# Kernel tuning notes

Measured on AMD Instinct MI355X. Metric: run time of the kernel, lower is better.

The kernel has to match this reference:

```python
import jax, jax.numpy as jnp
import numpy as np

SAMPLE_POINTS = 1000
THRESH = 0.1
MAX_RATIO = 0.1
BIG = 1e9


def _sobel_boundary(mask):
    # mask: [B, H, W] -> boundary magnitude [B, H, W]
    kx = jnp.array([[-1, 0, 1], [-2, 0, 2], [-1, 0, 1]], jnp.float32).reshape(1, 1, 3, 3)
    ky = jnp.array([[-1, -2, -1], [0, 0, 0], [1, 2, 1]], jnp.float32).reshape(1, 1, 3, 3)
    x = mask[:, None, :, :]
    dn = ('NCHW', 'OIHW', 'NCHW')
    gx = jax.lax.conv_general_dilated(x, kx, (1, 1), [(1, 1), (1, 1)], dimension_numbers=dn)
    gy = jax.lax.conv_general_dilated(x, ky, (1, 1), [(1, 1), (1, 1)], dimension_numbers=dn)
    return jnp.sqrt(gx * gx + gy * gy + 1e-8)[:, 0]


def _extract_points(bmap, keys, H, W):
    # bmap: [B, H, W]. Returns points [B, P, 2] float and validity mask [B, P].
    # Torch version uses torch.where + randperm subsampling; here we pick a
    # uniformly-random subset of valid boundary pixels via noisy top_k
    # (fixed-shape, jit-compatible stream compaction).
    def one(bm, key):
        flat = bm.reshape(-1)
        valid = flat > THRESH
        noise = jax.random.uniform(key, flat.shape)
        score = valid.astype(jnp.float32) * 2.0 + noise  # valid in (2,3), invalid in (0,1)
        _, idx = jax.lax.top_k(score, SAMPLE_POINTS)
        pts = jnp.stack([(idx // W).astype(jnp.float32), (idx % W).astype(jnp.float32)], axis=-1)
        pvalid = valid[idx]
        has_any = valid.any()
        # empty-boundary fallback: single center point (like torch version)
        center = jnp.array([H // 2, W // 2], jnp.float32)
        pts = jnp.where(has_any, pts, jnp.broadcast_to(center, pts.shape))
        pvalid = jnp.where(has_any, pvalid, jnp.arange(SAMPLE_POINTS) == 0)
        return pts, pvalid

    return jax.vmap(one)(bmap, keys)


def _hausdorff(pp, pv, tp, tv, diag):
    # pp: [B,P,2], tp: [B,T,2]; masked symmetric Hausdorff per batch element.
    pp2 = jnp.sum(pp * pp, -1)  # [B,P]
    tp2 = jnp.sum(tp * tp, -1)  # [B,T]
    d2 = pp2[:, :, None] + tp2[:, None, :] - 2.0 * jnp.einsum('bpc,btc->bpt', pp, tp)
    D = jnp.sqrt(jnp.maximum(d2, 0.0))  # [B,P,T]
    min_p2t = jnp.min(jnp.where(tv[:, None, :], D, BIG), axis=2)  # [B,P]
    a = jnp.max(jnp.where(pv, min_p2t, -BIG), axis=1)  # [B]
    min_t2p = jnp.min(jnp.where(pv[:, :, None], D, BIG), axis=1)  # [B,T]
    b = jnp.max(jnp.where(tv, min_t2p, -BIG), axis=1)  # [B]
    hd = jnp.maximum(a, b) / diag
    return jnp.clip(hd, 0.0, MAX_RATIO)


def setup_inputs() -> dict:
    key = jax.random.key(0)
    k1, k2 = jax.random.split(key)
    B, H, W = 64, 512, 512
    pred_logits = jax.random.normal(k1, (B, H, W), dtype=jnp.float32)
    target = (jax.random.uniform(k2, (B, H, W)) > 0.5).astype(jnp.float32)
    return {"pred_logits": pred_logits, "target": target}


def reference(pred_logits, target):
    B, H, W = pred_logits.shape
    pred_probs = jax.nn.sigmoid(pred_logits)
    bmap_pred = _sobel_boundary(pred_probs)
    bmap_tgt = _sobel_boundary(target)
    keys = jax.random.split(jax.random.key(1), 2 * B)
    pp, pv = _extract_points(bmap_pred, keys[:B], H, W)
    tp, tv = _extract_points(bmap_tgt, keys[B:], H, W)
    diag = jnp.sqrt(jnp.float32(H * H + W * W))
    hd = _hausdorff(pp, pv, tp, tv, diag)  # [B]
    return jnp.mean(hd)
```

## Files before the change

kernel.cpp:

```cpp
#include <hip/hip_runtime.h>
#include <stdint.h>


#define HH 512
#define WW 512
#define NPIX (HH * WW)
#define NSEL 1000
#define SLICE_CAP 320
#define CUTM (253u << 14)
#define BITCUT ((((253u << 15) - 1u)) << 9)
#define ROWS_PER 32

#if __has_builtin(__builtin_amdgcn_alignbit)
__device__ __forceinline__ uint32_t rotl32(uint32_t x, int r) {
  return __builtin_amdgcn_alignbit(x, x, (32 - r) & 31);
}
#else
__device__ __forceinline__ uint32_t rotl32(uint32_t x, int r) {
  return (x << r) | (x >> (32 - r));
}
#endif

template <int R>
__device__ __forceinline__ uint32_t rotlT(uint32_t x) {
  uint32_t d;
  asm("v_alignbit_b32 %0, %1, %1, %2" : "=v"(d) : "v"(x), "n"(32 - R));
  return d;
}

__device__ __forceinline__ void tf2x32(uint32_t k0, uint32_t k1,
                                       uint32_t c0, uint32_t c1,
                                       uint32_t& o0, uint32_t& o1) {
  uint32_t ks2 = k0 ^ k1 ^ 0x1BD11BDAu;
  uint32_t x0 = c0 + k0, x1 = c1 + k1;
#define TF_R(r) { x0 += x1; x1 = rotl32(x1, (r)); x1 ^= x0; }
  TF_R(13) TF_R(15) TF_R(26) TF_R(6)
  x0 += k1;  x1 += ks2 + 1u;
  TF_R(17) TF_R(29) TF_R(16) TF_R(24)
  x0 += ks2; x1 += k0 + 2u;
  TF_R(13) TF_R(15) TF_R(26) TF_R(6)
  x0 += k0;  x1 += k1 + 3u;
  TF_R(17) TF_R(29) TF_R(16) TF_R(24)
  x0 += k1;  x1 += ks2 + 4u;
  TF_R(13) TF_R(15) TF_R(26) TF_R(6)
  x0 += ks2; x1 += k0 + 5u;
#undef TF_R
  o0 = x0; o1 = x1;
}

__device__ __forceinline__ uint32_t m_from_bits(uint32_t bits) {
  float noise = __uint_as_float((bits >> 9) | 0x3F800000u) - 1.0f;
  float score = 2.0f + noise;
  return __float_as_uint(score) - 0x40000000u;
}

__device__ __forceinline__ uint32_t pixel_m(uint32_t k0, uint32_t k1, int p) {
  uint32_t b1, b2;
  tf2x32(k0, k1, 0u, (uint32_t)p, b1, b2);
  return m_from_bits(b1 ^ b2);
}

__device__ __forceinline__ float sigf(float x) { return 1.0f / (1.0f + __expf(-x)); }

__device__ __forceinline__ float ldval(const float* __restrict__ img, int r, int c, bool isPred) {
  if (r < 0 || r > HH - 1 || c < 0 || c > WW - 1) return 0.0f;
  float v = img[(size_t)r * WW + c];
  return isPred ? sigf(v) : v;
}

__device__ __forceinline__ uint32_t pack_pt(uint32_t p) {
  return ((p >> 9) << 16) | (p & 511u);
}

template <bool PRED>
__device__ __forceinline__ void sobel_body(const float* __restrict__ img, int b,
                                           int slice, int t,
                                           unsigned long long* stage, int* s_cn,
                                           int* s_cv) {
  const int lane = t & 63, w = t >> 6;
  const int rbase = slice * ROWS_PER + 8 * w;
  uint32_t k0, k1;
  tf2x32(0u, 1u, 0u, (uint32_t)b, k0, k1);
  k0 = __builtin_amdgcn_readfirstlane(k0);
  k1 = __builtin_amdgcn_readfirstlane(k1);
  const uint32_t ks2 = k0 ^ k1 ^ 0x1BD11BDAu;

  float P[10], Q[10], R[10];
  float4 na, nb;
  int cnt = 0;
  const uint32_t pbase = (uint32_t)((rbase << 9) + (lane << 3));

  auto issue = [&](int rn) {
    if ((unsigned)rn < (unsigned)HH) {
      const float* rp = img + ((size_t)rn << 9) + (lane << 3);
      na = *(const float4*)rp;
      nb = *(const float4*)(rp + 4);
    }
  };
  auto promote = [&](float (&vv)[10], int rn) {
    if ((unsigned)rn < (unsigned)HH) {
      float4 x = na, y = nb;
      if (PRED) {
        x.x = sigf(x.x); x.y = sigf(x.y); x.z = sigf(x.z); x.w = sigf(x.w);
        y.x = sigf(y.x); y.y = sigf(y.y); y.z = sigf(y.z); y.w = sigf(y.w);
      }
      vv[1] = x.x; vv[2] = x.y; vv[3] = x.z; vv[4] = x.w;
      vv[5] = y.x; vv[6] = y.y; vv[7] = y.z; vv[8] = y.w;
      float l = __shfl_up(y.w, 1);
      float r = __shfl_down(x.x, 1);
      vv[0] = (lane == 0) ? 0.0f : l;
      vv[9] = (lane == 63) ? 0.0f : r;
    } else {
#pragma unroll
      for (int i = 0; i < 10; ++i) vv[i] = 0.0f;
    }
  };

  issue(rbase - 1); promote(P, rbase - 1);
  issue(rbase);     promote(Q, rbase);
  issue(rbase + 1);

#pragma unroll 1
  for (int r = 0; r < 8; ++r) {
    promote(R, rbase + r + 1);
    if (r < 7) issue(rbase + r + 2);
    __builtin_amdgcn_sched_barrier(0);

    const uint32_t prow = pbase + ((uint32_t)r << 9);
    uint32_t X0[8], X1[8];
    const uint32_t pk = prow + k1;
    const uint32_t s0 = pk + k0;
#pragma unroll
    for (int j = 0; j < 8; ++j) {
      uint32_t x1i = pk + (uint32_t)j;
      X0[j] = s0 + (uint32_t)j;
      X1[j] = rotlT<13>(x1i) ^ X0[j];
    }
#define RND(rr)                                                         \
  _Pragma("unroll") for (int j = 0; j < 8; ++j) {                       \
    X0[j] += X1[j];                                                     \
    X1[j] = rotlT<(rr)>(X1[j]) ^ X0[j];                                 \
  }
#define INJ(ka, kb, i)                                                  \
  _Pragma("unroll") for (int j = 0; j < 8; ++j) {                       \
    X0[j] += (ka);                                                      \
    X1[j] += (kb) + (uint32_t)(i);                                      \
  }
    RND(15) RND(26) RND(6)  INJ(k1, ks2, 1)
    RND(17) RND(29) RND(16) RND(24) INJ(ks2, k0, 2)
    RND(13) RND(15) RND(26) RND(6)  INJ(k0, k1, 3)
    RND(17) RND(29) RND(16) RND(24) INJ(k1, ks2, 4)
    RND(13) RND(15) RND(26) RND(6)  INJ(ks2, k0, 5)
#undef RND
#undef INJ
    uint32_t bits[8];
#pragma unroll
    for (int j = 0; j < 8; ++j) bits[j] = X0[j] ^ X1[j];

    float da[10], e[10];
#pragma unroll
    for (int k = 0; k < 10; ++k) {
      da[k] = R[k] - P[k];
      e[k] = P[k] + 2.0f * Q[k] + R[k];
    }
    uint32_t candmask = 0;
#pragma unroll
    for (int j = 0; j < 8; ++j) {
      float gx = e[j + 2] - e[j];
      float gy = da[j] + 2.0f * da[j + 1] + da[j + 2];
      bool vld = (gx * gx + gy * gy + 1e-8f) > 0.01f;
      cnt += vld ? 1 : 0;
      candmask |= ((vld && bits[j] >= BITCUT) ? 1u : 0u) << j;
    }
    if (candmask) {
      int base = atomicAdd(s_cn, __popc(candmask));
      do {
        int j = __ffs(candmask) - 1;
        candmask &= candmask - 1;
        if (base < SLICE_CAP) {
          uint32_t m = m_from_bits(bits[j]);
          stage[base] = ((unsigned long long)m << 32) | (prow + (uint32_t)j);
        }
        ++base;
      } while (candmask);
    }
#pragma unroll
    for (int k = 0; k < 10; ++k) { P[k] = Q[k]; Q[k] = R[k]; }
  }
#pragma unroll
  for (int o = 32; o > 0; o >>= 1) cnt += __shfl_down(cnt, o);
  if (lane == 0) atomicAdd(s_cv, cnt);
}

__global__ __launch_bounds__(256, 8) void sobel_cand(
    const float* __restrict__ pred, const float* __restrict__ tgt,
    int2* __restrict__ g_scnt, unsigned long long* __restrict__ g_cand,
    uint32_t* __restrict__ g_hmax, int* __restrict__ g_done) {
  const int bid = blockIdx.x;
  const int b = bid >> 4, s = bid & 15;
  const int t = threadIdx.x;
  __shared__ unsigned long long stage[SLICE_CAP];
  __shared__ int s_cn, s_cv;
  if (t == 0) { s_cn = 0; s_cv = 0; }
  if (bid == 0) {
    if (t < 64) g_hmax[t] = 0u;
    if (t == 64) *g_done = 0;
  }
  __syncthreads();
  if (b < 64) sobel_body<true>(pred + (size_t)b * NPIX, b, s, t, stage, &s_cn, &s_cv);
  else        sobel_body<false>(tgt + (size_t)(b - 64) * NPIX, b, s, t, stage, &s_cn, &s_cv);
  __syncthreads();
  const int raw = s_cn;
  const int n = raw < SLICE_CAP ? raw : SLICE_CAP;
  for (int i = t; i < n; i += 256) g_cand[(size_t)bid * SLICE_CAP + i] = stage[i];
  if (t == 0) g_scnt[bid] = make_int2(s_cv, raw);
}

__global__ __launch_bounds__(256) void resolve_kernel(
    const float* __restrict__ pred, const float* __restrict__ tgt,
    const int2* __restrict__ g_scnt, unsigned long long* __restrict__ g_cand,
    uint32_t* __restrict__ g_pts, int* __restrict__ g_counts) {
  const int img = blockIdx.x;
  const int t = threadIdx.x;

  __shared__ unsigned long long cand_s[16 * SLICE_CAP];
  __shared__ int segc[16];
  __shared__ int s_scx[16], s_scy[16];
  __shared__ int s_info[4];
  __shared__ int ch[256];
  __shared__ int fh[1024];
  __shared__ int aux[256];
  __shared__ unsigned long long ties[256];
  __shared__ int s_pos, s_nt, s_T1, s_r1, s_T2, s_r2, s_n;

  if (t < 16) {
    int2 v = g_scnt[img * 16 + t];
    s_scx[t] = v.x; s_scy[t] = v.y;
    segc[t] = v.y < SLICE_CAP ? v.y : SLICE_CAP;
  }
  if (t == 0) { s_pos = 0; s_nt = 0; s_n = 0; }
  __syncthreads();
  if (t == 0) {
    int cv = 0, hi = 0, ovf = 0;
    for (int s = 0; s < 16; ++s) {
      cv += s_scx[s]; hi += s_scy[s];
      if (s_scy[s] > SLICE_CAP) ovf = 1;
    }
    s_info[0] = cv; s_info[1] = hi; s_info[2] = ovf;
  }
  __syncthreads();
  const int cv = s_info[0];
  if (cv == 0) {
    if (t == 0) { g_pts[img * NSEL] = (256u << 16) | 256u; g_counts[img] = 1; }
    return;
  }
  const int need = cv < NSEL ? cv : NSEL;
  bool slow = (s_info[2] != 0) || (s_info[1] < need);

  unsigned long long* C = g_cand + (size_t)img * 16 * SLICE_CAP;
  int ncand = 0;

  if (slow) {
    const bool isPred = img < 64;
    const float* im = isPred ? pred + (size_t)img * NPIX : tgt + (size_t)(img - 64) * NPIX;
    uint32_t k0, k1;
    tf2x32(0u, 1u, 0u, (uint32_t)img, k0, k1);
    ch[t] = 0;
    __syncthreads();
    for (int p = t; p < NPIX; p += 256) {
      int r = p >> 9, c = p & 511;
      float gx = (ldval(im, r - 1, c + 1, isPred) - ldval(im, r - 1, c - 1, isPred)) +
                 2.0f * (ldval(im, r, c + 1, isPred) - ldval(im, r, c - 1, isPred)) +
                 (ldval(im, r + 1, c + 1, isPred) - ldval(im, r + 1, c - 1, isPred));
      float gy = (ldval(im, r + 1, c - 1, isPred) - ldval(im, r - 1, c - 1, isPred)) +
                 2.0f * (ldval(im, r + 1, c, isPred) - ldval(im, r - 1, c, isPred)) +
                 (ldval(im, r + 1, c + 1, isPred) - ldval(im, r - 1, c + 1, isPred));
      if ((gx * gx + gy * gy + 1e-8f) > 0.01f) {
        uint32_t m = pixel_m(k0, k1, p);
        uint32_t cb = m >> 14; if (cb > 255u) cb = 255u;
        atomicAdd(&ch[cb], 1);
      }
    }
    __syncthreads();
    {
      aux[t] = ch[t];
      __syncthreads();
      for (int o = 1; o < 256; o <<= 1) {
        int v = (t + o < 256) ? aux[t + o] : 0;
        __syncthreads();
        aux[t] += v;
        __syncthreads();
      }
      int nx = (t + 1 < 256) ? aux[t + 1] : 0;
      if (aux[t] >= need && nx < need) s_T1 = t;
      __syncthreads();
    }
    const uint32_t Tc = (uint32_t)s_T1;
    if (t == 0) s_info[3] = 0;
    __syncthreads();
    for (int p = t; p < NPIX; p += 256) {
      int r = p >> 9, c = p & 511;
      float gx = (ldval(im, r - 1, c + 1, isPred) - ldval(im, r - 1, c - 1, isPred)) +
                 2.0f * (ldval(im, r, c + 1, isPred) - ldval(im, r, c - 1, isPred)) +
                 (ldval(im, r + 1, c + 1, isPred) - ldval(im, r + 1, c - 1, isPred));
      float gy = (ldval(im, r + 1, c - 1, isPred) - ldval(im, r - 1, c - 1, isPred)) +
                 2.0f * (ldval(im, r + 1, c, isPred) - ldval(im, r - 1, c, isPred)) +
                 (ldval(im, r + 1, c + 1, isPred) - ldval(im, r - 1, c + 1, isPred));
      if ((gx * gx + gy * gy + 1e-8f) > 0.01f) {
        uint32_t m = pixel_m(k0, k1, p);
        uint32_t cb = m >> 14; if (cb > 255u) cb = 255u;
        if (cb >= Tc) {
          int i = atomicAdd(&s_info[3], 1);
          if (i < 16 * SLICE_CAP) C[i] = ((unsigned long long)m << 32) | (uint32_t)p;
        }
      }
    }
    __syncthreads();
    ncand = s_info[3] < 16 * SLICE_CAP ? s_info[3] : 16 * SLICE_CAP;
  }

  if (slow) {
    for (int i = t; i < ncand; i += 256) cand_s[i] = C[i];
    if (t == 0) s_n = ncand;
  } else {
    for (int i = t; i < 16 * SLICE_CAP; i += 256) {
      int s = i / SLICE_CAP;
      int o = i - s * SLICE_CAP;
      if (o < segc[s]) {
        unsigned long long e = C[i];
        cand_s[atomicAdd(&s_n, 1)] = e;
      }
    }
  }
  ch[t] = 0;
  for (int i = t; i < 1024; i += 256) fh[i] = 0;
  __syncthreads();
  const int n = s_n;

  for (int i = t; i < n; i += 256) {
    uint32_t m = (uint32_t)(cand_s[i] >> 32);
    uint32_t cb = m >> 14; if (cb > 255u) cb = 255u;
    atomicAdd(&ch[cb], 1);
  }
  __syncthreads();
  {
    aux[t] = ch[t];
    __syncthreads();
    for (int o = 1; o < 256; o <<= 1) {
      int v = (t + o < 256) ? aux[t + o] : 0;
      __syncthreads();
      aux[t] += v;
      __syncthreads();
    }
    int nx = (t + 1 < 256) ? aux[t + 1] : 0;
    if (aux[t] >= need && nx < need) { s_T1 = t; s_r1 = need - nx; }
    __syncthreads();
  }
  const uint32_t T1 = (uint32_t)s_T1;
  const int r1 = s_r1;
  const uint32_t baseM = T1 << 14;

  for (int i = t; i < n; i += 256) {
    unsigned long long e = cand_s[i];
    uint32_t m = (uint32_t)(e >> 32), p = (uint32_t)e;
    uint32_t cb = m >> 14; if (cb > 255u) cb = 255u;
    if (cb > T1) {
      int pos = atomicAdd(&s_pos, 1);
      g_pts[img * NSEL + pos] = pack_pt(p);
    } else if (cb == T1) {
      uint32_t f = (m - baseM) >> 4; if (f > 1023u) f = 1023u;
      atomicAdd(&fh[f], 1);
    }
  }
  __syncthreads();
  {
    int base = 4 * t, sv = 0;
    for (int j = 3; j >= 0; --j) { sv += fh[base + j]; fh[base + j] = sv; }
    aux[t] = sv;
    __syncthreads();
    for (int o = 1; o < 256; o <<= 1) {
      int v = (t + o < 256) ? aux[t + o] : 0;
      __syncthreads();
      aux[t] += v;
      __syncthreads();
    }
    int add = (t < 255) ? aux[t + 1] : 0;
    for (int j = 0; j < 4; ++j) fh[base + j] += add;
    __syncthreads();
    for (int j = 0; j < 4; ++j) {
      int idx = base + j;
      int sfx = fh[idx];
      int nx = (idx < 1023) ? fh[idx + 1] : 0;
      if (sfx >= r1 && nx < r1) { s_T2 = idx; s_r2 = r1 - nx; }
    }
    __syncthreads();
  }
  const int T2 = s_T2, r2 = s_r2;
  for (int i = t; i < n; i += 256) {
    unsigned long long e = cand_s[i];
    uint32_t m = (uint32_t)(e >> 32), p = (uint32_t)e;
    uint32_t cb = m >> 14; if (cb > 255u) cb = 255u;
    if (cb == T1) {
      uint32_t f = (m - baseM) >> 4; if (f > 1023u) f = 1023u;
      if ((int)f > T2) {
        int pos = atomicAdd(&s_pos, 1);
        g_pts[img * NSEL + pos] = pack_pt(p);
      } else if ((int)f == T2) {
        int j = atomicAdd(&s_nt, 1);
        if (j < 256) ties[j] = e;
      }
    }
  }
  __syncthreads();
  int nt = s_nt < 256 ? s_nt : 256;
  for (int i = t; i < nt; i += 256) {
    unsigned long long e = ties[i];
    uint32_t mi = (uint32_t)(e >> 32), pi = (uint32_t)e;
    int rank = 0;
    for (int j = 0; j < nt; ++j) {
      unsigned long long e2 = ties[j];
      uint32_t mj = (uint32_t)(e2 >> 32), pj = (uint32_t)e2;
      rank += (mj > mi) || (mj == mi && pj < pi);
    }
    if (rank < r2) {
      int pos = atomicAdd(&s_pos, 1);
      g_pts[img * NSEL + pos] = pack_pt(pi);
    }
  }
  __syncthreads();
  if (t == 0) g_counts[img] = s_pos;
}

__global__ __launch_bounds__(256) void haus_kernel(
    const uint32_t* __restrict__ g_pts, const int* __restrict__ g_counts,
    uint32_t* __restrict__ g_hmax, int* __restrict__ g_done,
    float* __restrict__ out) {
  const int bid = blockIdx.x;
  const int img = bid >> 3;
  const int dir = (bid >> 2) & 1;
  const int seg = bid & 3;
  const int t = threadIdx.x;
  const int iOwn = dir ? 64 + img : img;
  const int iOth = dir ? img : 64 + img;
  const int nOwn = g_counts[iOwn];
  const int nOth = g_counts[iOth];
  __shared__ float2 o[NSEL];
  __shared__ float red[256];
  __shared__ int s_ticket;
  for (int i = t; i < nOth; i += 256) {
    uint32_t v = g_pts[iOth * NSEL + i];
    o[i] = make_float2((float)(v >> 16), (float)(v & 0xFFFFu));
  }
  __syncthreads();
  float best = 0.0f;
  const int lo = seg * 250;
  const int hi = min(nOwn, lo + 250);
  for (int i = lo + t; i < hi; i += 256) {
    uint32_t v = g_pts[iOwn * NSEL + i];
    float pr = (float)(v >> 16), pc = (float)(v & 0xFFFFu);
    float mn0 = 3.4e38f, mn1 = 3.4e38f, mn2 = 3.4e38f, mn3 = 3.4e38f;
    int j = 0;
    for (; j + 3 < nOth; j += 4) {
      float dr0 = pr - o[j].x,     dc0 = pc - o[j].y;
      float dr1 = pr - o[j + 1].x, dc1 = pc - o[j + 1].y;
      float dr2 = pr - o[j + 2].x, dc2 = pc - o[j + 2].y;
      float dr3 = pr - o[j + 3].x, dc3 = pc - o[j + 3].y;
      mn0 = fminf(mn0, dr0 * dr0 + dc0 * dc0);
      mn1 = fminf(mn1, dr1 * dr1 + dc1 * dc1);
      mn2 = fminf(mn2, dr2 * dr2 + dc2 * dc2);
      mn3 = fminf(mn3, dr3 * dr3 + dc3 * dc3);
    }
    for (; j < nOth; ++j) {
      float dr = pr - o[j].x, dc = pc - o[j].y;
      mn0 = fminf(mn0, dr * dr + dc * dc);
    }
    float mn = fminf(fminf(mn0, mn1), fminf(mn2, mn3));
    best = fmaxf(best, mn);
  }
  red[t] = best;
  __syncthreads();
  for (int st = 128; st > 0; st >>= 1) {
    if (t < st) red[t] = fmaxf(red[t], red[t + st]);
    __syncthreads();
  }
  if (t == 0) {
    atomicMax(&g_hmax[img], __float_as_uint(red[0]));
    __threadfence();
    s_ticket = atomicAdd(g_done, 1);
  }
  __syncthreads();
  if (s_ticket == 511) {
    __threadfence();
    if (t < 64) {
      uint32_t u = atomicMax(&g_hmax[t], 0u);
      float diag = sqrtf((float)(HH * HH + WW * WW));
      float hd = sqrtf(fmaxf(__uint_as_float(u), 0.0f)) / diag;
      hd = fminf(fmaxf(hd, 0.0f), 0.1f);
      float s = hd;
      for (int o2 = 32; o2 > 0; o2 >>= 1) s += __shfl_down(s, o2);
      if (t == 0) out[0] = s * 0.015625f;
    }
  }
}

#define WS_SCNT   0u
#define WS_COUNTS 16384u
#define WS_HMAX   (WS_COUNTS + 512u)
#define WS_DONE   (WS_HMAX + 256u)
#define WS_PTS    (WS_HMAX + 2048u)
#define WS_CAND   (WS_PTS + 512000u)

extern "C" void kernel_launch(void* const* d_in, const int* in_sizes, int n_in,
                              void* d_out, int out_size, void* d_ws, size_t ws_size,
                              hipStream_t stream) {
  const float* pred = (const float*)d_in[0];
  const float* tgt = (const float*)d_in[1];
  float* out = (float*)d_out;
  char* ws = (char*)d_ws;
  int2* g_scnt = (int2*)(ws + WS_SCNT);
  int* g_counts = (int*)(ws + WS_COUNTS);
  uint32_t* g_hmax = (uint32_t*)(ws + WS_HMAX);
  int* g_done = (int*)(ws + WS_DONE);
  uint32_t* g_pts = (uint32_t*)(ws + WS_PTS);
  unsigned long long* g_cand = (unsigned long long*)(ws + WS_CAND);

  sobel_cand<<<2048, 256, 0, stream>>>(pred, tgt, g_scnt, g_cand, g_hmax, g_done);
  resolve_kernel<<<128, 256, 0, stream>>>(pred, tgt, g_scnt, g_cand, g_pts, g_counts);
  haus_kernel<<<512, 256, 0, stream>>>(g_pts, g_counts, g_hmax, g_done, out);
}
```

Before: 245.6 us.

## Widen resolve kernel to 1024 threads with wave-aggregated atomics and prefix-sum compaction

```diff
diff --git a/kernel.cpp b/kernel.cpp
--- a/kernel.cpp
+++ b/kernel.cpp
@@ -10,6 +10,7 @@
 #define CUTM (253u << 14)
 #define BITCUT ((((253u << 15) - 1u)) << 9)
 #define ROWS_PER 32
+#define K2_BS 1024
 
 #if __has_builtin(__builtin_amdgcn_alignbit)
 __device__ __forceinline__ uint32_t rotl32(uint32_t x, int r) {
@@ -192,7 +193,7 @@
   if (lane == 0) atomicAdd(s_cv, cnt);
 }
 
-__global__ __launch_bounds__(256, 8) void sobel_cand(
+__global__ __launch_bounds__(256, 4) void sobel_cand(
     const float* __restrict__ pred, const float* __restrict__ tgt,
     int2* __restrict__ g_scnt, unsigned long long* __restrict__ g_cand,
     uint32_t* __restrict__ g_hmax, int* __restrict__ g_done) {
@@ -216,15 +217,16 @@
   if (t == 0) g_scnt[bid] = make_int2(s_cv, raw);
 }
 
-__global__ __launch_bounds__(256) void resolve_kernel(
+__global__ __launch_bounds__(K2_BS) void resolve_kernel(
     const float* __restrict__ pred, const float* __restrict__ tgt,
     const int2* __restrict__ g_scnt, unsigned long long* __restrict__ g_cand,
     uint32_t* __restrict__ g_pts, int* __restrict__ g_counts) {
   const int img = blockIdx.x;
   const int t = threadIdx.x;
+  const int lane = t & 63;
 
   __shared__ unsigned long long cand_s[16 * SLICE_CAP];
-  __shared__ int segc[16];
+  __shared__ int segc[16], segoff[17];
   __shared__ int s_scx[16], s_scy[16];
   __shared__ int s_info[4];
   __shared__ int ch[256];
@@ -238,14 +240,17 @@
     s_scx[t] = v.x; s_scy[t] = v.y;
     segc[t] = v.y < SLICE_CAP ? v.y : SLICE_CAP;
   }
-  if (t == 0) { s_pos = 0; s_nt = 0; s_n = 0; }
+  if (t == 0) { s_pos = 0; s_nt = 0; }
   __syncthreads();
   if (t == 0) {
-    int cv = 0, hi = 0, ovf = 0;
+    int cv = 0, hi = 0, ovf = 0, off = 0;
     for (int s = 0; s < 16; ++s) {
       cv += s_scx[s]; hi += s_scy[s];
       if (s_scy[s] > SLICE_CAP) ovf = 1;
-    }
+      segoff[s] = off; off += segc[s];
+    }
+    segoff[16] = off;
+    s_n = off;
     s_info[0] = cv; s_info[1] = hi; s_info[2] = ovf;
   }
   __syncthreads();
@@ -255,19 +260,18 @@
     return;
   }
   const int need = cv < NSEL ? cv : NSEL;
-  bool slow = (s_info[2] != 0) || (s_info[1] < need);
+  const bool slow = (s_info[2] != 0) || (s_info[1] < need);
 
   unsigned long long* C = g_cand + (size_t)img * 16 * SLICE_CAP;
-  int ncand = 0;
 
   if (slow) {
     const bool isPred = img < 64;
     const float* im = isPred ? pred + (size_t)img * NPIX : tgt + (size_t)(img - 64) * NPIX;
     uint32_t k0, k1;
     tf2x32(0u, 1u, 0u, (uint32_t)img, k0, k1);
-    ch[t] = 0;
-    __syncthreads();
-    for (int p = t; p < NPIX; p += 256) {
+    if (t < 256) ch[t] = 0;
+    __syncthreads();
+    for (int p = t; p < NPIX; p += K2_BS) {
       int r = p >> 9, c = p & 511;
       float gx = (ldval(im, r - 1, c + 1, isPred) - ldval(im, r - 1, c - 1, isPred)) +
                  2.0f * (ldval(im, r, c + 1, isPred) - ldval(im, r, c - 1, isPred)) +
@@ -282,23 +286,24 @@
       }
     }
     __syncthreads();
-    {
-      aux[t] = ch[t];
+    if (t < 256) aux[t] = ch[t];
+    __syncthreads();
+    for (int o = 1; o < 256; o <<= 1) {
+      int v = 0;
+      if (t < 256 && t + o < 256) v = aux[t + o];
       __syncthreads();
-      for (int o = 1; o < 256; o <<= 1) {
-        int v = (t + o < 256) ? aux[t + o] : 0;
-        __syncthreads();
-        aux[t] += v;
-        __syncthreads();
-      }
+      if (t < 256) aux[t] += v;
+      __syncthreads();
+    }
+    if (t < 256) {
       int nx = (t + 1 < 256) ? aux[t + 1] : 0;
       if (aux[t] >= need && nx < need) s_T1 = t;
-      __syncthreads();
-    }
+    }
+    __syncthreads();
     const uint32_t Tc = (uint32_t)s_T1;
     if (t == 0) s_info[3] = 0;
     __syncthreads();
-    for (int p = t; p < NPIX; p += 256) {
+    for (int p = t; p < NPIX; p += K2_BS) {
       int r = p >> 9, c = p & 511;
       float gx = (ldval(im, r - 1, c + 1, isPred) - ldval(im, r - 1, c - 1, isPred)) +
                  2.0f * (ldval(im, r, c + 1, isPred) - ldval(im, r, c - 1, isPred)) +
@@ -316,104 +321,134 @@
       }
     }
     __syncthreads();
-    ncand = s_info[3] < 16 * SLICE_CAP ? s_info[3] : 16 * SLICE_CAP;
-  }
-
-  if (slow) {
-    for (int i = t; i < ncand; i += 256) cand_s[i] = C[i];
-    if (t == 0) s_n = ncand;
+    if (t == 0) s_n = s_info[3] < 16 * SLICE_CAP ? s_info[3] : 16 * SLICE_CAP;
+    __syncthreads();
+  }
+
+  {
+    const int nn = s_n;
+    if (slow) {
+      for (int i = t; i < nn; i += K2_BS) cand_s[i] = C[i];
+    } else {
+      for (int i = t; i < 16 * SLICE_CAP; i += K2_BS) {
+        int s = i / SLICE_CAP;
+        int o = i - s * SLICE_CAP;
+        if (o < segc[s]) cand_s[segoff[s] + o] = C[i];
+      }
+    }
+  }
+  if (t < 256) ch[t] = 0;
+  fh[t] = 0;
+  __syncthreads();
+  const int n = s_n;
+
+  if (!slow) {
+    int l0 = 0, l1 = 0, l2 = 0;
+    for (int i = t; i < n; i += K2_BS) {
+      uint32_t cb = (uint32_t)(cand_s[i] >> 32) >> 14; if (cb > 255u) cb = 255u;
+      if (cb == 253u) ++l0; else if (cb == 254u) ++l1; else ++l2;
+    }
+#pragma unroll
+    for (int o = 32; o > 0; o >>= 1) {
+      l0 += __shfl_down(l0, o); l1 += __shfl_down(l1, o); l2 += __shfl_down(l2, o);
+    }
+    if (lane == 0) {
+      if (l0) atomicAdd(&ch[253], l0);
+      if (l1) atomicAdd(&ch[254], l1);
+      if (l2) atomicAdd(&ch[255], l2);
+    }
   } else {
-    for (int i = t; i < 16 * SLICE_CAP; i += 256) {
-      int s = i / SLICE_CAP;
-      int o = i - s * SLICE_CAP;
-      if (o < segc[s]) {
-        unsigned long long e = C[i];
-        cand_s[atomicAdd(&s_n, 1)] = e;
-      }
-    }
-  }
-  ch[t] = 0;
-  for (int i = t; i < 1024; i += 256) fh[i] = 0;
-  __syncthreads();
-  const int n = s_n;
-
-  for (int i = t; i < n; i += 256) {
-    uint32_t m = (uint32_t)(cand_s[i] >> 32);
-    uint32_t cb = m >> 14; if (cb > 255u) cb = 255u;
-    atomicAdd(&ch[cb], 1);
-  }
-  __syncthreads();
-  {
-    aux[t] = ch[t];
-    __syncthreads();
-    for (int o = 1; o < 256; o <<= 1) {
-      int v = (t + o < 256) ? aux[t + o] : 0;
-      __syncthreads();
-      aux[t] += v;
-      __syncthreads();
-    }
+    for (int i = t; i < n; i += K2_BS) {
+      uint32_t cb = (uint32_t)(cand_s[i] >> 32) >> 14; if (cb > 255u) cb = 255u;
+      atomicAdd(&ch[cb], 1);
+    }
+  }
+  __syncthreads();
+  if (t < 256) aux[t] = ch[t];
+  __syncthreads();
+  for (int o = 1; o < 256; o <<= 1) {
+    int v = 0;
+    if (t < 256 && t + o < 256) v = aux[t + o];
+    __syncthreads();
+    if (t < 256) aux[t] += v;
+    __syncthreads();
+  }
+  if (t < 256) {
     int nx = (t + 1 < 256) ? aux[t + 1] : 0;
     if (aux[t] >= need && nx < need) { s_T1 = t; s_r1 = need - nx; }
-    __syncthreads();
-  }
+  }
+  __syncthreads();
   const uint32_t T1 = (uint32_t)s_T1;
   const int r1 = s_r1;
   const uint32_t baseM = T1 << 14;
 
-  for (int i = t; i < n; i += 256) {
-    unsigned long long e = cand_s[i];
+  for (int base = 0; base < n; base += K2_BS) {
+    const int i = base + t;
+    const bool in = i < n;
+    unsigned long long e = in ? cand_s[i] : 0ull;
     uint32_t m = (uint32_t)(e >> 32), p = (uint32_t)e;
     uint32_t cb = m >> 14; if (cb > 255u) cb = 255u;
-    if (cb > T1) {
-      int pos = atomicAdd(&s_pos, 1);
-      g_pts[img * NSEL + pos] = pack_pt(p);
-    } else if (cb == T1) {
+    bool emit = in && cb > T1;
+    unsigned long long msk = __ballot(emit);
+    if (msk) {
+      int leader = __ffsll(msk) - 1;
+      int bpos = 0;
+      if (lane == leader) bpos = atomicAdd(&s_pos, __popcll(msk));
+      bpos = __shfl(bpos, leader);
+      if (emit)
+        g_pts[img * NSEL + bpos + __popcll(msk & ((1ull << lane) - 1ull))] = pack_pt(p);
+    }
+    if (in && cb == T1) {
       uint32_t f = (m - baseM) >> 4; if (f > 1023u) f = 1023u;
       atomicAdd(&fh[f], 1);
     }
   }
   __syncthreads();
+  for (int o = 1; o < 1024; o <<= 1) {
+    int v = (t + o < 1024) ? fh[t + o] : 0;
+    __syncthreads();
+    fh[t] += v;
+    __syncthreads();
+  }
   {
-    int base = 4 * t, sv = 0;
-    for (int j = 3; j >= 0; --j) { sv += fh[base + j]; fh[base + j] = sv; }
-    aux[t] = sv;
-    __syncthreads();
-    for (int o = 1; o < 256; o <<= 1) {
-      int v = (t + o < 256) ? aux[t + o] : 0;
-      __syncthreads();
-      aux[t] += v;
-      __syncthreads();
-    }
-    int add = (t < 255) ? aux[t + 1] : 0;
-    for (int j = 0; j < 4; ++j) fh[base + j] += add;
-    __syncthreads();
-    for (int j = 0; j < 4; ++j) {
-      int idx = base + j;
-      int sfx = fh[idx];
-      int nx = (idx < 1023) ? fh[idx + 1] : 0;
-      if (sfx >= r1 && nx < r1) { s_T2 = idx; s_r2 = r1 - nx; }
-    }
-    __syncthreads();
-  }
+    int nx = (t < 1023) ? fh[t + 1] : 0;
+    if (fh[t] >= r1 && nx < r1) { s_T2 = t; s_r2 = r1 - nx; }
+  }
+  __syncthreads();
   const int T2 = s_T2, r2 = s_r2;
-  for (int i = t; i < n; i += 256) {
-    unsigned long long e = cand_s[i];
+
+  for (int base = 0; base < n; base += K2_BS) {
+    const int i = base + t;
+    const bool in = i < n;
+    unsigned long long e = in ? cand_s[i] : 0ull;
     uint32_t m = (uint32_t)(e >> 32), p = (uint32_t)e;
     uint32_t cb = m >> 14; if (cb > 255u) cb = 255u;
-    if (cb == T1) {
-      uint32_t f = (m - baseM) >> 4; if (f > 1023u) f = 1023u;
-      if ((int)f > T2) {
-        int pos = atomicAdd(&s_pos, 1);
-        g_pts[img * NSEL + pos] = pack_pt(p);
-      } else if ((int)f == T2) {
-        int j = atomicAdd(&s_nt, 1);
-        if (j < 256) ties[j] = e;
-      }
-    }
-  }
-  __syncthreads();
-  int nt = s_nt < 256 ? s_nt : 256;
-  for (int i = t; i < nt; i += 256) {
+    uint32_t f = (m - baseM) >> 4; if (f > 1023u) f = 1023u;
+    const bool isT1 = in && cb == T1;
+    bool emit = isT1 && (int)f > T2;
+    bool tie  = isT1 && (int)f == T2;
+    unsigned long long msk = __ballot(emit);
+    if (msk) {
+      int leader = __ffsll(msk) - 1;
+      int bpos = 0;
+      if (lane == leader) bpos = atomicAdd(&s_pos, __popcll(msk));
+      bpos = __shfl(bpos, leader);
+      if (emit)
+        g_pts[img * NSEL + bpos + __popcll(msk & ((1ull << lane) - 1ull))] = pack_pt(p);
+    }
+    unsigned long long mt = __ballot(tie);
+    if (mt) {
+      int leader = __ffsll(mt) - 1;
+      int bpos = 0;
+      if (lane == leader) bpos = atomicAdd(&s_nt, __popcll(mt));
+      bpos = __shfl(bpos, leader);
+      int idx = bpos + __popcll(mt & ((1ull << lane) - 1ull));
+      if (tie && idx < 256) ties[idx] = e;
+    }
+  }
+  __syncthreads();
+  const int nt = s_nt < 256 ? s_nt : 256;
+  for (int i = t; i < nt; i += K2_BS) {
     unsigned long long e = ties[i];
     uint32_t mi = (uint32_t)(e >> 32), pi = (uint32_t)e;
     int rank = 0;
@@ -525,6 +560,6 @@
   unsigned long long* g_cand = (unsigned long long*)(ws + WS_CAND);
 
   sobel_cand<<<2048, 256, 0, stream>>>(pred, tgt, g_scnt, g_cand, g_hmax, g_done);
-  resolve_kernel<<<128, 256, 0, stream>>>(pred, tgt, g_scnt, g_cand, g_pts, g_counts);
+  resolve_kernel<<<128, K2_BS, 0, stream>>>(pred, tgt, g_scnt, g_cand, g_pts, g_counts);
   haus_kernel<<<512, 256, 0, stream>>>(g_pts, g_counts, g_hmax, g_done, out);
 }
```

Result: faster. 233.4 us (-5.0%).
